# Kernel tuning notes

Hardware: AMD Instinct MI355X
Metric: run time of the kernel (lower is better)

The kernel has to match this reference:

```python
import jax, jax.numpy as jnp
import numpy as np

TEMPERATURE = 0.07


def setup_inputs() -> dict:
    key = jax.random.key(0)
    k1, k2 = jax.random.split(key)
    B, V, C, H, W = 4, 2, 128, 32, 32
    features = jax.random.normal(k1, (B, V, C, H, W), dtype=jnp.float32)
    # L2-normalize per-pixel feature vectors (channel dim), as contrastive
    # embeddings are in practice; the original exp() is unstabilized.
    features = features / jnp.linalg.norm(features, axis=2, keepdims=True)
    labels = jax.random.randint(k2, (B, V, H, W), 0, 4, dtype=jnp.int32)
    return {"features": features, "labels": labels}


def reference(features, labels):
    B, V, C, H, W = features.shape
    # torch.cat(torch.unbind(features, dim=1), dim=0): views stacked along batch
    cf = jnp.transpose(features, (1, 0, 2, 3, 4)).reshape(B * V, C, H, W)
    # kernels = cf.permute(0,2,3,1).reshape(-1, C, 1, 1); conv2d with 1x1 kernels
    # == pairwise dot products of per-pixel feature vectors.
    X = jnp.transpose(cf, (0, 2, 3, 1)).reshape(-1, C)  # [N, C], N = B*V*H*W
    N = X.shape[0]
    logits = (X @ X.T) / TEMPERATURE  # [N, N]

    lab = jnp.transpose(labels, (1, 0, 2, 3)).reshape(-1)  # [N]
    mask = (lab[:, None] == lab[None, :]).astype(logits.dtype)  # [N, N]
    logits_mask = 1.0 - jnp.eye(N, dtype=logits.dtype)  # zero the diagonal
    mask = mask * logits_mask

    exp_logits = jnp.exp(logits) * logits_mask
    log_prob = logits - jnp.log(jnp.sum(exp_logits, axis=1, keepdims=True))
    mean_log_prob_pos = jnp.sum(mask * log_prob, axis=1) / jnp.sum(mask, axis=1)
    loss = -mean_log_prob_pos  # [N]

    non_bg = (lab != 0).astype(logits.dtype)
    return jnp.sum(loss * non_bg) / jnp.sum(non_bg)
```

## Files before the change

kernel.cpp:

```cpp
#include <hip/hip_runtime.h>
#include <hip/hip_bf16.h>
#include <stdint.h>

typedef short bf16x8 __attribute__((ext_vector_type(8)));
typedef float f32x16 __attribute__((ext_vector_type(16)));

#define NROWS 8192
#define CDIM  128
#define TEMP  0.07f
#define C1F   20.6099291555566248f

#define OFF_S     2097152
#define OFF_SUM   2129920
#define OFF_TKT   2129924
#define OFF_G     2129984
#define OFF_HIST  2132032
#define OFF_GPART 2132096
#define OFF_HPART 2656384
#define ZWORDS    8194

__device__ __forceinline__ float bf2f(unsigned short u) {
  union { unsigned int i; float f; } x; x.i = ((unsigned int)u) << 16; return x.f;
}
__device__ __forceinline__ unsigned short f2bf(float f) {
  union { float f; unsigned int i; } x; x.f = f;
  unsigned int r = x.i + 0x7fffu + ((x.i >> 16) & 1u);
  return (unsigned short)(r >> 16);
}
__device__ __forceinline__ float fexp2(float x) {
#if __has_builtin(__builtin_amdgcn_exp2f)
  return __builtin_amdgcn_exp2f(x);
#else
  return exp2f(x);
#endif
}

__global__ __launch_bounds__(256) void k_pack(const float* __restrict__ F,
                                              const int* __restrict__ labels,
                                              char* __restrict__ ws) {
  unsigned short* Xb    = (unsigned short*)ws;
  float*          zbase = (float*)(ws + OFF_S);
  float*          Gpart = (float*)(ws + OFF_GPART);
  int*            Hpart = (int*)(ws + OFF_HPART);

  __shared__ float lds[128 * 33];
  __shared__ float gp[2][4][128];
  __shared__ int   lab_lds[32];

  const int tid = threadIdx.x;
  const int bid = blockIdx.x;

  {
    int idx = bid * 256 + tid;
    if (idx < ZWORDS) zbase[idx] = 0.0f;
  }

  const int g   = bid >> 5;
  const int hw0 = (bid & 31) << 5;
  const int n0  = g * 1024 + hw0;
  if (tid < 32) lab_lds[tid] = labels[n0 + tid];

#pragma unroll
  for (int p = 0; p < 16; ++p) {
    int c  = p * 8 + (tid >> 5);
    int hw = hw0 + (tid & 31);
    lds[c * 33 + (tid & 31)] = F[(g * 128 + c) * 1024 + hw];
  }
  __syncthreads();

  const int c = tid & 127;
  const int h = tid >> 7;
  float a0 = 0.f, a1 = 0.f, a2 = 0.f, a3 = 0.f;
#pragma unroll
  for (int p = 0; p < 16; ++p) {
    int hwl = p * 2 + h;
    float vf = lds[c * 33 + hwl];
    unsigned short vb = f2bf(vf);
    Xb[(n0 + hwl) * 128 + c] = vb;
    float v  = bf2f(vb);
    int  lab = lab_lds[hwl];
    a0 += (lab == 0) ? v : 0.f;
    a1 += (lab == 1) ? v : 0.f;
    a2 += (lab == 2) ? v : 0.f;
    a3 += (lab == 3) ? v : 0.f;
  }
  gp[h][0][c] = a0; gp[h][1][c] = a1; gp[h][2][c] = a2; gp[h][3][c] = a3;
  __syncthreads();
  if (tid < 128) {
#pragma unroll
    for (int l = 0; l < 4; ++l)
      Gpart[bid * 512 + l * 128 + tid] = gp[0][l][tid] + gp[1][l][tid];
  }
  if (tid < 4) {
    int hh = 0;
#pragma unroll
    for (int r = 0; r < 32; ++r) hh += (lab_lds[r] == tid);
    Hpart[bid * 4 + tid] = hh;
  }
}

__global__ __launch_bounds__(256, 2) void k_main(const unsigned short* __restrict__ Xb,
                                                 char* __restrict__ ws) {
  float* S     = (float*)(ws + OFF_S);
  float* Gpart = (float*)(ws + OFF_GPART);
  int*   Hpart = (int*)(ws + OFF_HPART);
  float* G     = (float*)(ws + OFF_G);
  int*   hist  = (int*)(ws + OFF_HIST);

  const int bid = blockIdx.x;
  const int tid = threadIdx.x;

  if (bid >= 512) {
    const int rb2 = bid - 512;
    const int e   = rb2 * 128 + (tid >> 1);
    const int hh  = tid & 1;
    float s = 0.f;
    for (int b = hh * 128; b < hh * 128 + 128; ++b) s += Gpart[b * 512 + e];
    s += __shfl_xor(s, 1, 64);
    if (hh == 0) G[e] = s;
    if (rb2 == 0 && tid < 4) {
      int cth = 0;
      for (int b = 0; b < 256; ++b) cth += Hpart[b * 4 + tid];
      hist[tid] = cth;
    }
    return;
  }

  const int lane = tid & 63;
  const int wave = tid >> 6;
  const int m    = lane & 31;
  const int half = lane >> 5;
  const int rb   = bid >> 4;
  const int sp   = bid & 15;
  const int r0   = rb * 256 + wave * 64;
  const int col0 = sp * 512;

  bf16x8 afrag[2][8];
#pragma unroll
  for (int rs = 0; rs < 2; ++rs)
#pragma unroll
    for (int s = 0; s < 8; ++s)
      afrag[rs][s] = *(const bf16x8*)(Xb + (r0 + rs * 32 + m) * CDIM + half * 8 + s * 16);

  float accS0[16], accS1[16];
#pragma unroll
  for (int r = 0; r < 16; ++r) { accS0[r] = 0.f; accS1[r] = 0.f; }

  const unsigned short* bptr = Xb + (col0 + m) * CDIM + half * 8;
  bf16x8 bf[2][8];
#pragma unroll
  for (int s = 0; s < 8; ++s) bf[0][s] = *(const bf16x8*)(bptr + s * 16);

#pragma unroll 2
  for (int g = 0; g < 16; ++g) {
    const int p = g & 1;
    if (g < 15) {
      const unsigned short* np = bptr + (g + 1) * 32 * CDIM;
#pragma unroll
      for (int s = 0; s < 8; ++s) bf[p ^ 1][s] = *(const bf16x8*)(np + s * 16);
    }
    f32x16 a0, a1;
#pragma unroll
    for (int r = 0; r < 16; ++r) { a0[r] = 0.f; a1[r] = 0.f; }
#pragma unroll
    for (int s = 0; s < 8; ++s)
      a0 = __builtin_amdgcn_mfma_f32_32x32x16_bf16(afrag[0][s], bf[p][s], a0, 0, 0, 0);
#pragma unroll
    for (int s = 0; s < 8; ++s)
      a1 = __builtin_amdgcn_mfma_f32_32x32x16_bf16(afrag[1][s], bf[p][s], a1, 0, 0, 0);

    const int colbase = col0 + g * 32;
    if (r0 == colbase) {
      const int colg = colbase + m;
#pragma unroll
      for (int r = 0; r < 16; ++r) {
        int   row = r0 + (r & 3) + 8 * (r >> 2) + 4 * half;
        float arg = (row == colg) ? -1e30f : a0[r] * C1F;
        accS0[r] += fexp2(arg);
      }
    } else {
#pragma unroll
      for (int r = 0; r < 16; ++r) accS0[r] += fexp2(a0[r] * C1F);
    }
    if (r0 + 32 == colbase) {
      const int colg = colbase + m;
#pragma unroll
      for (int r = 0; r < 16; ++r) {
        int   row = r0 + 32 + (r & 3) + 8 * (r >> 2) + 4 * half;
        float arg = (row == colg) ? -1e30f : a1[r] * C1F;
        accS1[r] += fexp2(arg);
      }
    } else {
#pragma unroll
      for (int r = 0; r < 16; ++r) accS1[r] += fexp2(a1[r] * C1F);
    }
  }

#pragma unroll
  for (int r = 0; r < 16; ++r) {
    float v = accS0[r];
    v += __shfl_xor(v, 1, 64);  v += __shfl_xor(v, 2, 64);
    v += __shfl_xor(v, 4, 64);  v += __shfl_xor(v, 8, 64);
    v += __shfl_xor(v, 16, 64);
    accS0[r] = v;
    float w = accS1[r];
    w += __shfl_xor(w, 1, 64);  w += __shfl_xor(w, 2, 64);
    w += __shfl_xor(w, 4, 64);  w += __shfl_xor(w, 8, 64);
    w += __shfl_xor(w, 16, 64);
    accS1[r] = w;
  }
  if (m == 0) {
#pragma unroll
    for (int r = 0; r < 16; ++r) {
      int rr = (r & 3) + 8 * (r >> 2) + 4 * half;
      atomicAdd(&S[r0 + rr], accS0[r]);
      atomicAdd(&S[r0 + 32 + rr], accS1[r]);
    }
  }
}

__global__ __launch_bounds__(256) void k_loss(const unsigned short* __restrict__ Xb,
                                              const int* __restrict__ labels,
                                              char* __restrict__ ws,
                                              float* __restrict__ out) {
  const float* S       = (const float*)(ws + OFF_S);
  const float* G       = (const float*)(ws + OFF_G);
  const int*   hist    = (const int*)(ws + OFF_HIST);
  float*       sumLoss = (float*)(ws + OFF_SUM);
  int*         ticket  = (int*)(ws + OFF_TKT);

  const int i   = blockIdx.x * 256 + threadIdx.x;
  const int lab = labels[i];
  const float* gl = G + lab * 128;
  const unsigned short* x = Xb + i * CDIM;
  float dot = 0.f, nrm = 0.f;
#pragma unroll
  for (int cc = 0; cc < 16; ++cc) {
    int4 q = *(const int4*)(x + cc * 8);
    const unsigned int* qs = (const unsigned int*)&q;
#pragma unroll
    for (int j = 0; j < 4; ++j) {
      unsigned int u = qs[j];
      float lo = __uint_as_float(u << 16);
      float hi = __uint_as_float(u & 0xffff0000u);
      int   ci = cc * 8 + j * 2;
      dot += lo * gl[ci] + hi * gl[ci + 1];
      nrm += lo * lo + hi * hi;
    }
  }
  float Si   = S[i];
  float cnt  = (float)(hist[lab] - 1);
  float loss = logf(Si) - (dot - nrm) / (TEMP * cnt);
  float contrib = (lab != 0) ? loss : 0.f;
  for (int mm = 1; mm < 64; mm <<= 1) contrib += __shfl_xor(contrib, mm, 64);
  __shared__ float ws4[4];
  if ((threadIdx.x & 63) == 0) ws4[threadIdx.x >> 6] = contrib;
  __syncthreads();
  if (threadIdx.x == 0) {
    atomicAdd(sumLoss, ws4[0] + ws4[1] + ws4[2] + ws4[3]);
    __threadfence();
    int t = atomicAdd(ticket, 1);
    if (t == 31) {
      float total = atomicAdd(sumLoss, 0.0f);
      out[0] = total / (float)(NROWS - hist[0]);
    }
  }
}

extern "C" void kernel_launch(void* const* d_in, const int* in_sizes, int n_in,
                              void* d_out, int out_size, void* d_ws, size_t ws_size,
                              hipStream_t stream) {
  const float* F      = (const float*)d_in[0];
  const int*   labels = (const int*)d_in[1];
  char* ws = (char*)d_ws;
  unsigned short* Xb = (unsigned short*)ws;

  hipLaunchKernelGGL(k_pack, dim3(256), dim3(256), 0, stream, F, labels, ws);
  hipLaunchKernelGGL(k_main, dim3(516), dim3(256), 0, stream, Xb, ws);
  hipLaunchKernelGGL(k_loss, dim3(32), dim3(256), 0, stream, Xb, labels, ws,
                     (float*)d_out);
}
```

Before: 113.4 us.

## Exploit Gram matrix symmetry by computing only upper-triangular tiles

Replaces the full N×N exp-sum sweep with a triangular grid of 128×128 tiles, so each off-diagonal tile contributes both row sums and column sums through extra atomics. This roughly halves MFMA and exp work. B tiles are now staged through double-buffered LDS shared by four waves, instead of every wave loading them into registers, and the launch bound is raised to four blocks. The cost is more atomic traffic on S, an index computation using sqrt to find the tile, and smaller tiles with more blocks.

```diff
diff --git a/kernel.cpp b/kernel.cpp
--- a/kernel.cpp
+++ b/kernel.cpp
@@ -18,6 +18,10 @@
 #define OFF_GPART 2132096
 #define OFF_HPART 2656384
 #define ZWORDS    8194
+
+#define NTB   64
+#define NTRI  2080
+#define TAILB 4
 
 __device__ __forceinline__ float bf2f(unsigned short u) {
   union { unsigned int i; float f; } x; x.i = ((unsigned int)u) << 16; return x.f;
@@ -99,8 +103,8 @@
   }
 }
 
-__global__ __launch_bounds__(256, 2) void k_main(const unsigned short* __restrict__ Xb,
-                                                 char* __restrict__ ws) {
+__global__ __launch_bounds__(256, 4) void k_tri(const unsigned short* __restrict__ Xb,
+                                                char* __restrict__ ws) {
   float* S     = (float*)(ws + OFF_S);
   float* Gpart = (float*)(ws + OFF_GPART);
   int*   Hpart = (int*)(ws + OFF_HPART);
@@ -110,111 +114,127 @@
   const int bid = blockIdx.x;
   const int tid = threadIdx.x;
 
-  if (bid >= 512) {
-    const int rb2 = bid - 512;
-    const int e   = rb2 * 128 + (tid >> 1);
-    const int hh  = tid & 1;
+  if (bid < TAILB) {
+    const int e  = bid * 128 + (tid >> 1);
+    const int hh = tid & 1;
     float s = 0.f;
     for (int b = hh * 128; b < hh * 128 + 128; ++b) s += Gpart[b * 512 + e];
     s += __shfl_xor(s, 1, 64);
     if (hh == 0) G[e] = s;
-    if (rb2 == 0 && tid < 4) {
+    if (bid == 0 && tid < 4) {
       int cth = 0;
       for (int b = 0; b < 256; ++b) cth += Hpart[b * 4 + tid];
       hist[tid] = cth;
     }
     return;
   }
+
+  const int b = bid - TAILB;
+  int rb = (int)((129.0f - sqrtf((float)(129 * 129 - 8 * b))) * 0.5f);
+  if (rb < 0) rb = 0;
+  if (rb > 63) rb = 63;
+#define TRIBASE(r) ((r) * 64 - ((r) * ((r) - 1)) / 2)
+  while (rb > 0 && TRIBASE(rb) > b) --rb;
+  while (TRIBASE(rb + 1) <= b) ++rb;
+  const int cb   = rb + (b - TRIBASE(rb));
+  const bool diag = (rb == cb);
+
+  __shared__ int4 ldsB[2][528];
 
   const int lane = tid & 63;
   const int wave = tid >> 6;
   const int m    = lane & 31;
   const int half = lane >> 5;
-  const int rb   = bid >> 4;
-  const int sp   = bid & 15;
-  const int r0   = rb * 256 + wave * 64;
-  const int col0 = sp * 512;
-
-  bf16x8 afrag[2][8];
-#pragma unroll
-  for (int rs = 0; rs < 2; ++rs)
-#pragma unroll
-    for (int s = 0; s < 8; ++s)
-      afrag[rs][s] = *(const bf16x8*)(Xb + (r0 + rs * 32 + m) * CDIM + half * 8 + s * 16);
-
-  float accS0[16], accS1[16];
-#pragma unroll
-  for (int r = 0; r < 16; ++r) { accS0[r] = 0.f; accS1[r] = 0.f; }
-
-  const unsigned short* bptr = Xb + (col0 + m) * CDIM + half * 8;
-  bf16x8 bf[2][8];
-#pragma unroll
-  for (int s = 0; s < 8; ++s) bf[0][s] = *(const bf16x8*)(bptr + s * 16);
-
-#pragma unroll 2
-  for (int g = 0; g < 16; ++g) {
-    const int p = g & 1;
-    if (g < 15) {
-      const unsigned short* np = bptr + (g + 1) * 32 * CDIM;
-#pragma unroll
-      for (int s = 0; s < 8; ++s) bf[p ^ 1][s] = *(const bf16x8*)(np + s * 16);
-    }
-    f32x16 a0, a1;
-#pragma unroll
-    for (int r = 0; r < 16; ++r) { a0[r] = 0.f; a1[r] = 0.f; }
-#pragma unroll
-    for (int s = 0; s < 8; ++s)
-      a0 = __builtin_amdgcn_mfma_f32_32x32x16_bf16(afrag[0][s], bf[p][s], a0, 0, 0, 0);
-#pragma unroll
-    for (int s = 0; s < 8; ++s)
-      a1 = __builtin_amdgcn_mfma_f32_32x32x16_bf16(afrag[1][s], bf[p][s], a1, 0, 0, 0);
-
-    const int colbase = col0 + g * 32;
+  const int r0   = rb * 128 + wave * 32;
+  const int c0   = cb * 128;
+
+  bf16x8 afrag[8];
+#pragma unroll
+  for (int s = 0; s < 8; ++s)
+    afrag[s] = *(const bf16x8*)(Xb + (r0 + m) * CDIM + (half + 2 * s) * 8);
+
+  float accS[16];
+#pragma unroll
+  for (int r = 0; r < 16; ++r) accS[r] = 0.f;
+  float colAcc[4];
+
+  const int n_l = tid >> 3;
+  const int bq  = tid & 7;
+  const unsigned short* src = Xb + (c0 + n_l) * CDIM + bq * 16;
+  int4 v0 = *(const int4*)src;
+  int4 v1 = *(const int4*)(src + 8);
+  ldsB[0][(2 * bq) * 33 + n_l]     = v0;
+  ldsB[0][(2 * bq + 1) * 33 + n_l] = v1;
+  src += 32 * CDIM;
+  v0 = *(const int4*)src;
+  v1 = *(const int4*)(src + 8);
+
+#pragma unroll
+  for (int g = 0; g < 4; ++g) {
+    __syncthreads();
+    if (g < 3) {
+      const int nb = (g + 1) & 1;
+      ldsB[nb][(2 * bq) * 33 + n_l]     = v0;
+      ldsB[nb][(2 * bq + 1) * 33 + n_l] = v1;
+    }
+    if (g < 2) {
+      src += 32 * CDIM;
+      v0 = *(const int4*)src;
+      v1 = *(const int4*)(src + 8);
+    }
+    const int cur = g & 1;
+    f32x16 acc;
+#pragma unroll
+    for (int r = 0; r < 16; ++r) acc[r] = 0.f;
+#pragma unroll
+    for (int s = 0; s < 8; ++s) {
+      bf16x8 bfrag = *(const bf16x8*)&ldsB[cur][(half + 2 * s) * 33 + m];
+      acc = __builtin_amdgcn_mfma_f32_32x32x16_bf16(afrag[s], bfrag, acc, 0, 0, 0);
+    }
+    const int colbase = c0 + g * 32;
+    float csum = 0.f;
     if (r0 == colbase) {
-      const int colg = colbase + m;
 #pragma unroll
       for (int r = 0; r < 16; ++r) {
-        int   row = r0 + (r & 3) + 8 * (r >> 2) + 4 * half;
-        float arg = (row == colg) ? -1e30f : a0[r] * C1F;
-        accS0[r] += fexp2(arg);
+        int   rr  = (r & 3) + 8 * (r >> 2) + 4 * half;
+        float arg = (rr == m) ? -1e30f : acc[r] * C1F;
+        float e   = fexp2(arg);
+        accS[r] += e;
+        csum    += e;
       }
     } else {
 #pragma unroll
-      for (int r = 0; r < 16; ++r) accS0[r] += fexp2(a0[r] * C1F);
-    }
-    if (r0 + 32 == colbase) {
-      const int colg = colbase + m;
-#pragma unroll
       for (int r = 0; r < 16; ++r) {
-        int   row = r0 + 32 + (r & 3) + 8 * (r >> 2) + 4 * half;
-        float arg = (row == colg) ? -1e30f : a1[r] * C1F;
-        accS1[r] += fexp2(arg);
+        float e = fexp2(acc[r] * C1F);
+        accS[r] += e;
+        csum    += e;
       }
-    } else {
-#pragma unroll
-      for (int r = 0; r < 16; ++r) accS1[r] += fexp2(a1[r] * C1F);
-    }
+    }
+    colAcc[g] = csum;
   }
 
 #pragma unroll
   for (int r = 0; r < 16; ++r) {
-    float v = accS0[r];
+    float v = accS[r];
     v += __shfl_xor(v, 1, 64);  v += __shfl_xor(v, 2, 64);
     v += __shfl_xor(v, 4, 64);  v += __shfl_xor(v, 8, 64);
     v += __shfl_xor(v, 16, 64);
-    accS0[r] = v;
-    float w = accS1[r];
-    w += __shfl_xor(w, 1, 64);  w += __shfl_xor(w, 2, 64);
-    w += __shfl_xor(w, 4, 64);  w += __shfl_xor(w, 8, 64);
-    w += __shfl_xor(w, 16, 64);
-    accS1[r] = w;
+    accS[r] = v;
   }
   if (m == 0) {
 #pragma unroll
     for (int r = 0; r < 16; ++r) {
       int rr = (r & 3) + 8 * (r >> 2) + 4 * half;
-      atomicAdd(&S[r0 + rr], accS0[r]);
-      atomicAdd(&S[r0 + 32 + rr], accS1[r]);
+      atomicAdd(&S[r0 + rr], accS[r]);
+    }
+  }
+
+  if (!diag) {
+#pragma unroll
+    for (int g = 0; g < 4; ++g) {
+      float v = colAcc[g];
+      v += __shfl_xor(v, 32, 64);
+      if (half == 0) atomicAdd(&S[c0 + g * 32 + m], v);
     }
   }
 }
@@ -276,7 +296,7 @@
   unsigned short* Xb = (unsigned short*)ws;
 
   hipLaunchKernelGGL(k_pack, dim3(256), dim3(256), 0, stream, F, labels, ws);
-  hipLaunchKernelGGL(k_main, dim3(516), dim3(256), 0, stream, Xb, ws);
+  hipLaunchKernelGGL(k_tri, dim3(NTRI + TAILB), dim3(256), 0, stream, Xb, ws);
   hipLaunchKernelGGL(k_loss, dim3(32), dim3(256), 0, stream, Xb, labels, ws,
                      (float*)d_out);
 }
```

Result: faster. 103.5 us (-8.7%).
